# Optimization experiments

Measured on AMD Instinct MI355X. Metric: run time of the kernel, lower is better.

## Reference

```python
import jax, jax.numpy as jnp
import numpy as np

N, IN_DIM, HID, HEADS = 20000, 3000, 128, 4
S_DIM, P_DIM = 32, 32
E = 320000
NEG_SLOPE = 0.2
ETA = 1e-6


def _glorot(key, shape):
    fan_in, fan_out = shape[0], shape[-1] if len(shape) > 1 else shape[0]
    lim = np.sqrt(6.0 / (fan_in + fan_out))
    return jax.random.uniform(key, shape, jnp.float32, -lim, lim)


def _gat_params(key, in_dim, out_ch, heads, concat):
    k1, k2, k3 = jax.random.split(key, 3)
    Wl = _glorot(k1, (in_dim, heads * out_ch))
    Wr = _glorot(k2, (in_dim, heads * out_ch))
    att = _glorot(k3, (heads, out_ch))
    b = jnp.zeros((heads * out_ch,) if concat else (out_ch,), jnp.float32)
    return Wl, Wr, att, b


def setup_inputs() -> dict:
    key = jax.random.key(0)
    ks = jax.random.split(key, 6)
    x = jax.random.normal(ks[0], (N, IN_DIM), jnp.float32)
    edge_index = jax.random.randint(ks[1], (2, E), 0, N, jnp.int32)
    out = {"x": x, "edge_index": edge_index}
    for name, kk, (ind, oc, h, cc) in [
        ("s1", ks[2], (IN_DIM, HID, HEADS, True)),
        ("s2", ks[3], (HID * HEADS, S_DIM * 2, 1, False)),
        ("p1", ks[4], (IN_DIM, HID, HEADS, True)),
        ("p2", ks[5], (HID * HEADS, P_DIM * 2, 1, False)),
    ]:
        Wl, Wr, att, b = _gat_params(kk, ind, oc, h, cc)
        out[f"Wl_{name}"] = Wl
        out[f"Wr_{name}"] = Wr
        out[f"att_{name}"] = att
        out[f"b_{name}"] = b
    return out


def gatv2(x, src, dst, Wl, Wr, att, b, heads, out_ch, concat):
    n = x.shape[0]
    xl = (x @ Wl).reshape(n, heads, out_ch)  # source transform
    xr = (x @ Wr).reshape(n, heads, out_ch)  # target transform
    m = xl[src]                                           # [E, H, C] messages
    e = jnp.sum(att * jax.nn.leaky_relu(m + xr[dst], NEG_SLOPE), axis=-1)  # [E, H]
    emax = jax.ops.segment_max(e, dst, num_segments=n)    # self-loops -> no empty segments
    ee = jnp.exp(e - emax[dst])
    denom = jax.ops.segment_sum(ee, dst, num_segments=n)
    alpha = ee / denom[dst]                               # segment softmax over incoming edges
    agg = jax.ops.segment_sum(m * alpha[..., None], dst, num_segments=n)  # [N, H, C]
    out = agg.reshape(n, heads * out_ch) if concat else agg.mean(axis=1)
    return out + b


def reference(x, edge_index, Wl_s1, Wr_s1, att_s1, b_s1, Wl_s2, Wr_s2, att_s2, b_s2,
              Wl_p1, Wr_p1, att_p1, b_p1, Wl_p2, Wr_p2, att_p2, b_p2):
    n = x.shape[0]
    loop = jnp.arange(n, dtype=edge_index.dtype)
    src = jnp.concatenate([edge_index[0], loop])  # add_self_loops (PyG default)
    dst = jnp.concatenate([edge_index[1], loop])
    s = jax.nn.relu(gatv2(x, src, dst, Wl_s1, Wr_s1, att_s1, b_s1, HEADS, HID, True))
    s = gatv2(s, src, dst, Wl_s2, Wr_s2, att_s2, b_s2, 1, S_DIM * 2, False)
    p = gatv2(x, src, dst, Wl_p1, Wr_p1, att_p1, b_p1, HEADS, HID, True)
    p = gatv2(p, src, dst, Wl_p2, Wr_p2, att_p2, b_p2, 1, P_DIM * 2, False)
    mu = jnp.concatenate([s[:, :S_DIM], p[:, :P_DIM]], axis=-1)
    sig = jnp.concatenate([jax.nn.softplus(s[:, S_DIM:]) + ETA,
                           jax.nn.softplus(p[:, P_DIM:]) + ETA], axis=-1)
    return mu, sig
```

## Files before the change

kernel.cpp:

```cpp
#include <hip/hip_runtime.h>
#include <cstdint>

#define NN     20000
#define NE     320000
#define ETOT   340000
#define K1R    3000
#define K1     3072
#define NPAD   20224
#define NCOL1  2048
#define LDA2   1024
#define MU_SZ  1280000

typedef __bf16 bf16x8 __attribute__((ext_vector_type(8)));
typedef float f32x4 __attribute__((ext_vector_type(4)));
typedef unsigned short u16x8 __attribute__((ext_vector_type(8)));

__device__ inline unsigned short f2bf(float f) {
  union { float f; unsigned u; } v; v.f = f;
  unsigned r = v.u + 0x7FFFu + ((v.u >> 16) & 1u);
  return (unsigned short)(r >> 16);
}
__device__ inline float bf2f(unsigned short h) {
  union { unsigned u; float f; } v; v.u = ((unsigned)h) << 16;
  return v.f;
}

typedef const __attribute__((address_space(1))) void* gas1_t;
typedef __attribute__((address_space(3))) void* las3_t;
__device__ inline void llds16(const void* g, void* l) {
  __builtin_amdgcn_global_load_lds((gas1_t)(uintptr_t)g,
                                   (las3_t)(uint32_t)(uintptr_t)l, 16, 0, 0);
}


__global__ __launch_bounds__(256)
void k_convert_x(const float* __restrict__ X, unsigned short* __restrict__ Xb) {
  const int CH = K1 / 8;
  int idx = blockIdx.x * 256 + threadIdx.x;
  if (idx >= NPAD * CH) return;
  int r = idx / CH, c8 = (idx % CH) * 8;
  u16x8 o;
  if (r < NN && c8 < K1R) {
    const float4* p = (const float4*)(X + (size_t)r * K1R + c8);
    float4 a = p[0], b = p[1];
    o[0]=f2bf(a.x); o[1]=f2bf(a.y); o[2]=f2bf(a.z); o[3]=f2bf(a.w);
    o[4]=f2bf(b.x); o[5]=f2bf(b.y); o[6]=f2bf(b.z); o[7]=f2bf(b.w);
  } else {
#pragma unroll
    for (int j = 0; j < 8; j++) o[j] = 0;
  }
  *(u16x8*)(Xb + (size_t)r * K1 + c8) = o;
}

__global__ __launch_bounds__(256)
void k_pack_w1(const float* __restrict__ W0, const float* __restrict__ W1,
               const float* __restrict__ W2, const float* __restrict__ W3,
               unsigned short* __restrict__ Wp) {
  __shared__ float tile[64][65];
  int k0 = blockIdx.x * 64, n0 = blockIdx.y * 64;
  int m = n0 >> 9, c0 = n0 & 511;
  const float* W = (m == 0) ? W0 : (m == 1) ? W1 : (m == 2) ? W2 : W3;
  int tx = threadIdx.x & 63, ty = threadIdx.x >> 6;
#pragma unroll
  for (int rep = 0; rep < 16; rep++) {
    int i = ty + rep * 4;
    int k = k0 + i;
    tile[i][tx] = (k < K1R) ? W[(size_t)k * 512 + c0 + tx] : 0.f;
  }
  __syncthreads();
#pragma unroll
  for (int rep = 0; rep < 16; rep++) {
    int i = ty + rep * 4;
    Wp[(size_t)(n0 + i) * K1 + k0 + tx] = f2bf(tile[tx][i]);
  }
}

__global__ __launch_bounds__(256)
void k_pack_w2(const float* __restrict__ Wl, const float* __restrict__ Wr,
               unsigned short* __restrict__ B2) {
  int idx = blockIdx.x * 256 + threadIdx.x;
  if (idx >= 128 * 1024) return;
  int n = idx >> 10, k = idx & 1023, kk = k & 511;
  float v = (n < 64) ? Wl[(size_t)kk * 64 + n] : Wr[(size_t)kk * 64 + (n - 64)];
  B2[idx] = f2bf(v);
}


__global__ __launch_bounds__(256)
void k_count(const int* __restrict__ ei, int* __restrict__ counts) {
  int e = blockIdx.x * 256 + threadIdx.x;
  if (e >= ETOT) return;
  int dst = (e < NE) ? ei[NE + e] : (e - NE);
  atomicAdd(&counts[dst], 1);
}

__global__ void k_scan(const int* __restrict__ counts, int* __restrict__ row_ptr) {
  __shared__ int part[1024];
  int t = threadIdx.x;
  int base = t * 20;
  int loc[20];
  int s = 0;
#pragma unroll
  for (int i = 0; i < 20; i++) {
    int idx = base + i;
    loc[i] = s;
    s += (idx < NN) ? counts[idx] : 0;
  }
  part[t] = s;
  __syncthreads();
  for (int off = 1; off < 1024; off <<= 1) {
    int v = (t >= off) ? part[t - off] : 0;
    __syncthreads();
    part[t] += v;
    __syncthreads();
  }
  int pre = (t > 0) ? part[t - 1] : 0;
#pragma unroll
  for (int i = 0; i < 20; i++) {
    int idx = base + i;
    if (idx <= NN) row_ptr[idx] = pre + loc[i];
  }
}

__global__ __launch_bounds__(256)
void k_scatter(const int* __restrict__ ei, const int* __restrict__ row_ptr,
               int* __restrict__ fill, int* __restrict__ csr_src) {
  int e = blockIdx.x * 256 + threadIdx.x;
  if (e >= ETOT) return;
  int s_, d_;
  if (e < NE) { s_ = ei[e]; d_ = ei[NE + e]; } else { s_ = d_ = e - NE; }
  int pos = row_ptr[d_] + atomicAdd(&fill[d_], 1);
  csr_src[pos] = s_;
}


#define NT1 48

#define STAGE_ONE do { \
  if (sctr < 4 * NT1) { \
    int ts_ = sctr >> 2, o_ = sctr & 3, sb_ = ts_ & 1; \
    const unsigned short* gb_; char* lb_; int rb_; \
    if (o_ == 0)      { gb_ = A; rb_ = bmBase;       lb_ = lds + (sb_*2+0)*16384; } \
    else if (o_ == 1) { gb_ = B; rb_ = bnBase;       lb_ = lds + 65536 + (sb_*2+0)*16384; } \
    else if (o_ == 2) { gb_ = B; rb_ = bnBase + 128; lb_ = lds + 65536 + (sb_*2+1)*16384; } \
    else              { gb_ = A; rb_ = bmBase + 128; lb_ = lds + (sb_*2+1)*16384; } \
    const unsigned short* g0_ = gb_ + (size_t)(rb_ + trow) * 3072 + ts_ * 64 + scol; \
    llds16(g0_, lb_ + wid * 1024); \
    llds16(g0_ + (size_t)64 * 3072, lb_ + 8192 + wid * 1024); \
    sctr++; \
  } \
} while (0)

#define BOUND do { \
  if (t < NT1 - 2)       asm volatile("s_waitcnt vmcnt(4)" ::: "memory"); \
  else if (t == NT1 - 2) asm volatile("s_waitcnt vmcnt(0)" ::: "memory"); \
} while (0)

#define RDA(DST, BASE) do { \
  _Pragma("unroll") \
  for (int mi = 0; mi < 2; mi++) { \
    int r_ = rw * 32 + mi * 16 + l15; \
    DST[0][mi] = *(const bf16x8*)((BASE) + r_ * 128 + sw0); \
    DST[1][mi] = *(const bf16x8*)((BASE) + r_ * 128 + sw1); \
  } \
} while (0)

#define RDB(BASE) do { \
  _Pragma("unroll") \
  for (int ni = 0; ni < 4; ni++) { \
    int r_ = cw * 64 + ni * 16 + l15; \
    bb[0][ni] = *(const bf16x8*)((BASE) + r_ * 128 + sw0); \
    bb[1][ni] = *(const bf16x8*)((BASE) + r_ * 128 + sw1); \
  } \
} while (0)

#define PH_PRE do { \
  asm volatile("" ::: "memory"); \
  __builtin_amdgcn_s_barrier(); \
  asm volatile("" ::: "memory"); \
  __builtin_amdgcn_s_setprio(1); \
} while (0)

#define PH_POST do { \
  __builtin_amdgcn_s_setprio(0); \
  asm volatile("" ::: "memory"); \
  __builtin_amdgcn_s_barrier(); \
  asm volatile("" ::: "memory"); \
} while (0)

#define MF(MH, NH, AV) do { \
  _Pragma("unroll") \
  for (int mi = 0; mi < 2; mi++) \
    _Pragma("unroll") \
    for (int ni = 0; ni < 4; ni++) { \
      acc[MH][NH][mi][ni] = __builtin_amdgcn_mfma_f32_16x16x32_bf16(AV[0][mi], bb[0][ni], acc[MH][NH][mi][ni], 0, 0, 0); \
      acc[MH][NH][mi][ni] = __builtin_amdgcn_mfma_f32_16x16x32_bf16(AV[1][mi], bb[1][ni], acc[MH][NH][mi][ni], 0, 0, 0); \
    } \
} while (0)

__global__ __launch_bounds__(512, 2)
void gemm256(const unsigned short* __restrict__ A, const unsigned short* __restrict__ B,
             unsigned short* __restrict__ C) {
  __shared__ char lds[131072];
  int tid = threadIdx.x, wid = tid >> 6, lane = tid & 63;
  int l15 = lane & 15;
  int rw = wid & 3, cw = wid >> 2;
  int bid = blockIdx.x;
  int swz = (bid & 7) * 79 + (bid >> 3);
  int bm = swz % 79, bn = swz / 79;
  int bmBase = bm * 256, bnBase = bn * 256;
  int trow = tid >> 3;
  int scol = ((tid & 7) ^ ((tid >> 3) & 7)) * 8;
  int sw0 = (((lane >> 4) + 0) ^ (lane & 7)) * 16;
  int sw1 = (((lane >> 4) + 4) ^ (lane & 7)) * 16;
  f32x4 acc[2][2][2][4] = {};

  int sctr = 0;
  for (int i = 0; i < 6; i++) STAGE_ONE;
  asm volatile("s_waitcnt vmcnt(4)" ::: "memory");
  __builtin_amdgcn_s_barrier();
  asm volatile("" ::: "memory");

  for (int t = 0; t < NT1; t++) {
    int buf = t & 1;
    const char* A0h = lds + (buf * 2 + 0) * 16384;
    const char* A1h = lds + (buf * 2 + 1) * 16384;
    const char* B0h = lds + 65536 + (buf * 2 + 0) * 16384;
    const char* B1h = lds + 65536 + (buf * 2 + 1) * 16384;
    bf16x8 a0[2][2], a1[2][2], bb[2][4];

    RDA(a0, A0h);
    RDB(B0h);
    STAGE_ONE;
    PH_PRE;
    MF(0, 0, a0);
    PH_POST;

    RDA(a1, A1h);
    STAGE_ONE;
    PH_PRE;
    MF(1, 0, a1);
    PH_POST;

    RDB(B1h);
    STAGE_ONE;
    PH_PRE;
    MF(1, 1, a1);
    PH_POST;

    STAGE_ONE;
    PH_PRE;
    MF(0, 1, a0);
    __builtin_amdgcn_s_setprio(0);
    asm volatile("" ::: "memory");
    BOUND;
    __builtin_amdgcn_s_barrier();
    asm volatile("" ::: "memory");
  }

  unsigned short (*sq)[128] = (unsigned short (*)[128])lds;
#pragma unroll
  for (int mh = 0; mh < 2; mh++)
#pragma unroll
    for (int nh = 0; nh < 2; nh++) {
      __syncthreads();
#pragma unroll
      for (int mi = 0; mi < 2; mi++)
#pragma unroll
        for (int ni = 0; ni < 4; ni++)
#pragma unroll
          for (int r = 0; r < 4; r++)
            sq[rw * 32 + mi * 16 + (lane >> 4) * 4 + r][cw * 64 + ni * 16 + l15] =
                f2bf(acc[mh][nh][mi][ni][r]);
      __syncthreads();
#pragma unroll
      for (int it = 0; it < 4; it++) {
        int idx = it * 512 + tid;
        int row = idx >> 4, ch = idx & 15;
        *(u16x8*)(C + (size_t)(bmBase + mh * 128 + row) * NCOL1 + bnBase + nh * 128 + ch * 8) =
            *(const u16x8*)&sq[row][ch * 8];
      }
    }
}


__global__ __launch_bounds__(256)
void gemm_l2(const unsigned short* __restrict__ As, const unsigned short* __restrict__ Bs,
             float* __restrict__ Cs,
             const unsigned short* __restrict__ Ap, const unsigned short* __restrict__ Bp,
             float* __restrict__ Cp) {
  const int K = LDA2, lda = LDA2, ldb = LDA2, ldc = 128, mreal = NN;
  const unsigned short* A = blockIdx.y ? Ap : As;
  const unsigned short* B = blockIdx.y ? Bp : Bs;
  float* C = blockIdx.y ? Cp : Cs;
  __shared__ char smem_raw[16384];
  unsigned short* sA = (unsigned short*)smem_raw;
  unsigned short* sB = sA + 128 * 32;
  int bm = blockIdx.x;
  int tid = threadIdx.x, wid = tid >> 6, lane = tid & 63;
  int wr = wid >> 1, wc = wid & 1;
  f32x4 acc[4][4] = {};

  int ar = 32 * wid + (lane >> 2);
  int acol = (lane & 3) * 8;
  const unsigned short* Ag = A + (size_t)(bm * 128 + ar) * lda + acol;
  const unsigned short* Bg = B + (size_t)ar * ldb + acol;
  unsigned short* la0 = sA + (wid * 2) * 512;
  unsigned short* lb0 = sB + (wid * 2) * 512;
  int frow = lane & 15, koff = (lane >> 4) * 8;

  for (int kt = 0; kt < K; kt += 32) {
    llds16(Ag + kt, la0);
    llds16(Ag + kt + (size_t)16 * lda, la0 + 512);
    llds16(Bg + kt, lb0);
    llds16(Bg + kt + (size_t)16 * ldb, lb0 + 512);
    __syncthreads();
    bf16x8 af[4], bfr[4];
#pragma unroll
    for (int mi = 0; mi < 4; mi++)
      af[mi] = *(const bf16x8*)(sA + (wr * 64 + mi * 16 + frow) * 32 + koff);
#pragma unroll
    for (int ni = 0; ni < 4; ni++)
      bfr[ni] = *(const bf16x8*)(sB + (wc * 64 + ni * 16 + frow) * 32 + koff);
#pragma unroll
    for (int mi = 0; mi < 4; mi++)
#pragma unroll
      for (int ni = 0; ni < 4; ni++)
        acc[mi][ni] = __builtin_amdgcn_mfma_f32_16x16x32_bf16(af[mi], bfr[ni], acc[mi][ni], 0, 0, 0);
    __syncthreads();
  }

#pragma unroll
  for (int mi = 0; mi < 4; mi++) {
    int grow0 = bm * 128 + wr * 64 + mi * 16 + (lane >> 4) * 4;
#pragma unroll
    for (int ni = 0; ni < 4; ni++) {
      int gcol = wc * 64 + ni * 16 + (lane & 15);
#pragma unroll
      for (int r = 0; r < 4; r++) {
        int grow = grow0 + r;
        if (grow < mreal) C[(size_t)grow * ldc + gcol] = acc[mi][ni][r];
      }
    }
  }
}


__global__ __launch_bounds__(256)
void edge_agg1(const unsigned short* __restrict__ XL1,
               const int* __restrict__ row_ptr, const int* __restrict__ csr_src,
               const float* __restrict__ att_s, const float* __restrict__ att_p,
               const float* __restrict__ b_s, const float* __restrict__ b_p,
               unsigned short* __restrict__ A2s, unsigned short* __restrict__ A2p) {
  int gw = (blockIdx.x * 256 + threadIdx.x) >> 6;
  if (gw >= NN * 2) return;
  int n = gw >> 1, br = gw & 1;
  int lane = threadIdx.x & 63;
  int cb = lane * 8;
  const float* att = br ? att_p : att_s;
  const float* bias = br ? b_p : b_s;
  float xr[8], at[8], agg[8];
  bf16x8 xrv = *(const bf16x8*)(XL1 + (size_t)n * NCOL1 + br * 1024 + 512 + cb);
#pragma unroll
  for (int j = 0; j < 8; j++) { xr[j] = (float)xrv[j]; at[j] = att[cb + j]; agg[j] = 0.f; }
  float M = -1e30f, S = 0.f;
  const size_t srcoff = (size_t)br * 1024 + cb;
  int pe = row_ptr[n + 1];
  for (int p = row_ptr[n]; p < pe; ++p) {
    int src = csr_src[p];
    bf16x8 mv = *(const bf16x8*)(XL1 + (size_t)src * NCOL1 + srcoff);
    float mj[8], part = 0.f;
#pragma unroll
    for (int j = 0; j < 8; j++) {
      mj[j] = (float)mv[j];
      float t = mj[j] + xr[j];
      t = (t > 0.f) ? t : 0.2f * t;
      part = fmaf(at[j], t, part);
    }
#pragma unroll
    for (int w = 1; w < 16; w <<= 1) part += __shfl_xor(part, w);
    float nm = fmaxf(M, part);
    float fac = __expf(M - nm);
    float wgt = __expf(part - nm);
    S = S * fac + wgt;
#pragma unroll
    for (int j = 0; j < 8; j++) agg[j] = agg[j] * fac + wgt * mj[j];
    M = nm;
  }
  float inv = 1.f / S;
  u16x8 hv, lv;
  unsigned short* A2 = br ? A2p : A2s;
#pragma unroll
  for (int j = 0; j < 8; j++) {
    float v = agg[j] * inv + bias[cb + j];
    if (!br) v = fmaxf(v, 0.f);
    unsigned short h = f2bf(v);
    float lo = v - bf2f(h);
    hv[j] = h; lv[j] = f2bf(lo);
  }
  *(u16x8*)(A2 + (size_t)n * LDA2 + cb) = hv;
  *(u16x8*)(A2 + (size_t)n * LDA2 + 512 + cb) = lv;
}


__global__ __launch_bounds__(256)
void edge_agg2(const float* __restrict__ C2s, const float* __restrict__ C2p,
               const int* __restrict__ row_ptr, const int* __restrict__ csr_src,
               const float* __restrict__ att_s, const float* __restrict__ att_p,
               const float* __restrict__ b_s, const float* __restrict__ b_p,
               float* __restrict__ out) {
  int gw = (blockIdx.x * 256 + threadIdx.x) >> 6;
  if (gw >= NN * 2) return;
  int n = gw >> 1, br = gw & 1;
  int lane = threadIdx.x & 63;
  const float* C2 = br ? C2p : C2s;
  float xr = C2[(size_t)n * 128 + 64 + lane];
  float at = (br ? att_p : att_s)[lane];
  float M = -1e30f, S = 0.f, agg = 0.f;
  int pe = row_ptr[n + 1];
  for (int p = row_ptr[n]; p < pe; ++p) {
    int src = csr_src[p];
    float m = C2[(size_t)src * 128 + lane];
    float t = m + xr;
    t = (t > 0.f) ? t : 0.2f * t;
    float part = at * t;
#pragma unroll
    for (int w = 1; w < 64; w <<= 1) part += __shfl_xor(part, w);
    float nm = fmaxf(M, part);
    float fac = __expf(M - nm);
    float wgt = __expf(part - nm);
    S = S * fac + wgt;
    agg = agg * fac + wgt * m;
    M = nm;
  }
  float v = agg / S + (br ? b_p : b_s)[lane];
  if (lane < 32) {
    out[(size_t)n * 64 + br * 32 + lane] = v;
  } else {
    float sp = fmaxf(v, 0.f) + log1pf(__expf(-fabsf(v))) + 1e-6f;
    out[(size_t)MU_SZ + n * 64 + br * 32 + (lane - 32)] = sp;
  }
}


extern "C" void kernel_launch(void* const* d_in, const int* in_sizes, int n_in,
                              void* d_out, int out_size, void* d_ws, size_t ws_size,
                              hipStream_t stream) {
  const float* x      = (const float*)d_in[0];
  const int*   ei     = (const int*)d_in[1];
  const float* Wl_s1  = (const float*)d_in[2];
  const float* Wr_s1  = (const float*)d_in[3];
  const float* att_s1 = (const float*)d_in[4];
  const float* b_s1   = (const float*)d_in[5];
  const float* Wl_s2  = (const float*)d_in[6];
  const float* Wr_s2  = (const float*)d_in[7];
  const float* att_s2 = (const float*)d_in[8];
  const float* b_s2   = (const float*)d_in[9];
  const float* Wl_p1  = (const float*)d_in[10];
  const float* Wr_p1  = (const float*)d_in[11];
  const float* att_p1 = (const float*)d_in[12];
  const float* b_p1   = (const float*)d_in[13];
  const float* Wl_p2  = (const float*)d_in[14];
  const float* Wr_p2  = (const float*)d_in[15];
  const float* att_p2 = (const float*)d_in[16];
  const float* b_p2   = (const float*)d_in[17];

  char* ws = (char*)d_ws;
  unsigned short* Xb   = (unsigned short*)(ws + 0);
  unsigned short* A2s  = (unsigned short*)(ws + 0);
  unsigned short* A2p  = (unsigned short*)(ws + 41156608);
  float*          C2s  = (float*)(ws + 82313216);
  float*          C2p  = (float*)(ws + 92553216);
  unsigned short* B2s  = (unsigned short*)(ws + 102793216);
  unsigned short* B2p  = (unsigned short*)(ws + 103055360);
  unsigned short* Wp   = (unsigned short*)(ws + 124256256);
  unsigned short* XL1  = (unsigned short*)(ws + 136839168);
  int* counts  = (int*)(ws + 219676672);
  int* fill    = (int*)(ws + 219756672);
  int* row_ptr = (int*)(ws + 219836672);
  int* csr_src = (int*)(ws + 219916688);

  hipMemsetAsync(counts, 0, NN * sizeof(int), stream);
  hipMemsetAsync(fill, 0, NN * sizeof(int), stream);

  k_convert_x<<<30336, 256, 0, stream>>>(x, Xb);
  k_pack_w1<<<dim3(48, 32), 256, 0, stream>>>(Wl_s1, Wr_s1, Wl_p1, Wr_p1, Wp);
  k_count<<<(ETOT + 255) / 256, 256, 0, stream>>>(ei, counts);
  k_scan<<<1, 1024, 0, stream>>>(counts, row_ptr);
  k_scatter<<<(ETOT + 255) / 256, 256, 0, stream>>>(ei, row_ptr, fill, csr_src);

  gemm256<<<632, 512, 0, stream>>>(Xb, Wp, XL1);

  k_pack_w2<<<512, 256, 0, stream>>>(Wl_s2, Wr_s2, B2s);
  k_pack_w2<<<512, 256, 0, stream>>>(Wl_p2, Wr_p2, B2p);

  edge_agg1<<<10000, 256, 0, stream>>>(XL1, row_ptr, csr_src, att_s1, att_p1, b_s1, b_p1, A2s, A2p);

  gemm_l2<<<dim3(157, 2), 256, 0, stream>>>(A2s, B2s, C2s, A2p, B2p, C2p);

  edge_agg2<<<10000, 256, 0, stream>>>(C2s, C2p, row_ptr, csr_src, att_s2, att_p2, b_s2, b_p2, (float*)d_out);
}
```

Before: 654.2 us.

## Simplify GEMM pipeline to one barrier per K-tile with full prefetch

```diff
diff --git a/kernel.cpp b/kernel.cpp
--- a/kernel.cpp
+++ b/kernel.cpp
@@ -151,11 +151,6 @@
   } \
 } while (0)
 
-#define BOUND do { \
-  if (t < NT1 - 2)       asm volatile("s_waitcnt vmcnt(4)" ::: "memory"); \
-  else if (t == NT1 - 2) asm volatile("s_waitcnt vmcnt(0)" ::: "memory"); \
-} while (0)
-
 #define RDA(DST, BASE) do { \
   _Pragma("unroll") \
   for (int mi = 0; mi < 2; mi++) { \
@@ -165,36 +160,22 @@
   } \
 } while (0)
 
-#define RDB(BASE) do { \
+#define RDB(DST, BASE) do { \
   _Pragma("unroll") \
   for (int ni = 0; ni < 4; ni++) { \
     int r_ = cw * 64 + ni * 16 + l15; \
-    bb[0][ni] = *(const bf16x8*)((BASE) + r_ * 128 + sw0); \
-    bb[1][ni] = *(const bf16x8*)((BASE) + r_ * 128 + sw1); \
+    DST[0][ni] = *(const bf16x8*)((BASE) + r_ * 128 + sw0); \
+    DST[1][ni] = *(const bf16x8*)((BASE) + r_ * 128 + sw1); \
   } \
 } while (0)
 
-#define PH_PRE do { \
-  asm volatile("" ::: "memory"); \
-  __builtin_amdgcn_s_barrier(); \
-  asm volatile("" ::: "memory"); \
-  __builtin_amdgcn_s_setprio(1); \
-} while (0)
-
-#define PH_POST do { \
-  __builtin_amdgcn_s_setprio(0); \
-  asm volatile("" ::: "memory"); \
-  __builtin_amdgcn_s_barrier(); \
-  asm volatile("" ::: "memory"); \
-} while (0)
-
-#define MF(MH, NH, AV) do { \
+#define MF(MH, NH, AV, BV) do { \
   _Pragma("unroll") \
   for (int mi = 0; mi < 2; mi++) \
     _Pragma("unroll") \
     for (int ni = 0; ni < 4; ni++) { \
-      acc[MH][NH][mi][ni] = __builtin_amdgcn_mfma_f32_16x16x32_bf16(AV[0][mi], bb[0][ni], acc[MH][NH][mi][ni], 0, 0, 0); \
-      acc[MH][NH][mi][ni] = __builtin_amdgcn_mfma_f32_16x16x32_bf16(AV[1][mi], bb[1][ni], acc[MH][NH][mi][ni], 0, 0, 0); \
+      acc[MH][NH][mi][ni] = __builtin_amdgcn_mfma_f32_16x16x32_bf16(AV[0][mi], BV[0][ni], acc[MH][NH][mi][ni], 0, 0, 0); \
+      acc[MH][NH][mi][ni] = __builtin_amdgcn_mfma_f32_16x16x32_bf16(AV[1][mi], BV[1][ni], acc[MH][NH][mi][ni], 0, 0, 0); \
     } \
 } while (0)
 
@@ -216,44 +197,29 @@
   f32x4 acc[2][2][2][4] = {};
 
   int sctr = 0;
-  for (int i = 0; i < 6; i++) STAGE_ONE;
-  asm volatile("s_waitcnt vmcnt(4)" ::: "memory");
+  for (int i = 0; i < 4; i++) STAGE_ONE;
+  asm volatile("s_waitcnt vmcnt(0)" ::: "memory");
   __builtin_amdgcn_s_barrier();
   asm volatile("" ::: "memory");
 
   for (int t = 0; t < NT1; t++) {
     int buf = t & 1;
+    STAGE_ONE; STAGE_ONE; STAGE_ONE; STAGE_ONE;
     const char* A0h = lds + (buf * 2 + 0) * 16384;
     const char* A1h = lds + (buf * 2 + 1) * 16384;
     const char* B0h = lds + 65536 + (buf * 2 + 0) * 16384;
     const char* B1h = lds + 65536 + (buf * 2 + 1) * 16384;
-    bf16x8 a0[2][2], a1[2][2], bb[2][4];
-
-    RDA(a0, A0h);
-    RDB(B0h);
-    STAGE_ONE;
-    PH_PRE;
-    MF(0, 0, a0);
-    PH_POST;
-
-    RDA(a1, A1h);
-    STAGE_ONE;
-    PH_PRE;
-    MF(1, 0, a1);
-    PH_POST;
-
-    RDB(B1h);
-    STAGE_ONE;
-    PH_PRE;
-    MF(1, 1, a1);
-    PH_POST;
-
-    STAGE_ONE;
-    PH_PRE;
-    MF(0, 1, a0);
+    bf16x8 a0[2][2], a1[2][2], b0[2][4], b1[2][4];
+    RDA(a0, A0h); RDA(a1, A1h);
+    RDB(b0, B0h); RDB(b1, B1h);
+    asm volatile("" ::: "memory");
+    __builtin_amdgcn_s_setprio(1);
+    MF(0, 0, a0, b0);
+    MF(1, 0, a1, b0);
+    MF(1, 1, a1, b1);
+    MF(0, 1, a0, b1);
     __builtin_amdgcn_s_setprio(0);
-    asm volatile("" ::: "memory");
-    BOUND;
+    asm volatile("s_waitcnt vmcnt(0)" ::: "memory");
     __builtin_amdgcn_s_barrier();
     asm volatile("" ::: "memory");
   }
```

New measurement: 631.6 us. 1.04x faster.
